# Optimization experiments

Hardware: AMD Instinct MI355X
Metric: run time of the kernel (lower is better)

Reference implementation:

```python
import jax, jax.numpy as jnp
import numpy as np

VAT_TOKENS = 57
ACTION_NUM = 56
NUM_HEADS = 16
DIM = 1152
HEAD_DIM = DIM // NUM_HEADS
SCALE = HEAD_DIM ** -0.5
N_GROUPS = 3  # num_non_act = 768 -> 3 groups of 256


def setup_inputs() -> dict:
    key = jax.random.key(0)
    ks = jax.random.split(key, 8)
    B, N, C = 32, VAT_TOKENS + 768, DIM
    w_std = C ** -0.5
    return {
        "x": jax.random.normal(ks[0], (B, N, C), jnp.float32),
        "w_qkv_non": jax.random.normal(ks[1], (3 * C, C), jnp.float32) * w_std,
        "w_q_act": jax.random.normal(ks[2], (C, C), jnp.float32) * w_std,
        "w_kv_act": jax.random.normal(ks[3], (2 * C, C), jnp.float32) * w_std,
        "w_proj_non": jax.random.normal(ks[4], (C, C), jnp.float32) * w_std,
        "b_proj_non": jnp.zeros((C,), jnp.float32),
        "w_proj_act": jax.random.normal(ks[5], (C, C), jnp.float32) * w_std,
        "b_proj_act": jnp.zeros((C,), jnp.float32),
    }


def reference(x, w_qkv_non, w_q_act, w_kv_act, w_proj_non, b_proj_non,
              w_proj_act, b_proj_act):
    B, N, C = x.shape
    H, Dh = NUM_HEADS, HEAD_DIM
    num_non_act = N - VAT_TOKENS
    G = num_non_act // N_GROUPS  # group size (256)

    # ---- non-action stream: windowed (grouped) self-attention ----
    non_act = x[:, VAT_TOKENS:]                                  # (B, 768, C)
    qkv = non_act @ w_qkv_non.T                                  # (B, 768, 3C)
    qkv = qkv.reshape(B, N_GROUPS, G, 3, H, Dh)
    q = qkv[:, :, :, 0]                                          # (B, g, G, H, Dh)
    k = qkv[:, :, :, 1]
    v = qkv[:, :, :, 2]
    attn = jnp.einsum('bgqhd,bgkhd->bghqk', q, k) * SCALE
    attn = jax.nn.softmax(attn, axis=-1)
    x_non = jnp.einsum('bghqk,bgkhd->bgqhd', attn, v)
    x_non = x_non.reshape(B, num_non_act, C)

    # ---- action stream: act queries attend to x[ACTION_NUM:] ----
    act = x[:, :VAT_TOKENS]
    q_act = (act @ w_q_act.T).reshape(B, VAT_TOKENS, H, Dh)
    kv = (x @ w_kv_act.T).reshape(B, N, 2, H, Dh)
    k_act = kv[:, ACTION_NUM:, 0]                                # (B, N-56, H, Dh)
    v_act = kv[:, ACTION_NUM:, 1]
    attn_act = jnp.einsum('bqhd,bkhd->bhqk', q_act, k_act) * SCALE
    attn_act = jax.nn.softmax(attn_act, axis=-1)
    x_act = jnp.einsum('bhqk,bkhd->bqhd', attn_act, v_act)
    x_act = x_act.reshape(B, VAT_TOKENS, C)

    # ---- output projections + concat ----
    x_non = x_non @ w_proj_non.T + b_proj_non
    x_act = x_act @ w_proj_act.T + b_proj_act
    return jnp.concatenate([x_act, x_non], axis=1)
```

## Files before the change

kernel.cpp:

```cpp
#include <hip/hip_runtime.h>

typedef __attribute__((ext_vector_type(8))) __bf16 bf16x8;
typedef __attribute__((ext_vector_type(4))) float f32x4;
typedef __attribute__((ext_vector_type(4))) unsigned short u16x4;
typedef __attribute__((ext_vector_type(8))) unsigned short u16x8;

#define MFMA_BF16 __builtin_amdgcn_mfma_f32_16x16x32_bf16

__device__ __forceinline__ unsigned short f2bf(float f) {
  union { float f; unsigned u; } v; v.f = f;
  unsigned r = v.u + 0x7FFFu + ((v.u >> 16) & 1u);
  return (unsigned short)(r >> 16);
}

__device__ __forceinline__ void gload16(const void* g, void* l) {
  __builtin_amdgcn_global_load_lds(
      (const __attribute__((address_space(1))) unsigned int*)g,
      (__attribute__((address_space(3))) unsigned int*)l, 16, 0, 0);
}

__global__ void __launch_bounds__(256) cast_bf16_kernel(const float* __restrict__ in,
                                                        unsigned short* __restrict__ out,
                                                        int n8) {
  int i = blockIdx.x * 256 + threadIdx.x;
  if (i >= n8) return;
  long base = (long)i * 8;
  float4 a = *(const float4*)(in + base);
  float4 b = *(const float4*)(in + base + 4);
  u16x8 o;
  o[0] = f2bf(a.x); o[1] = f2bf(a.y); o[2] = f2bf(a.z); o[3] = f2bf(a.w);
  o[4] = f2bf(b.x); o[5] = f2bf(b.y); o[6] = f2bf(b.z); o[7] = f2bf(b.w);
  *(u16x8*)(out + base) = o;
}

template <int REMAP>
__device__ __forceinline__ long remap_row(int m) {
  if (REMAP == 1) { int b = m / 768; return (long)b * 825 + 57 + (m - b * 768); }
  if (REMAP == 2) { int b = m / 57;  return (long)b * 825 + (m - b * 57); }
  return m;
}

template <int REMAP, bool PROJ>
__global__ void __launch_bounds__(512, 2) gemm256(const unsigned short* __restrict__ A,
                                                  const unsigned short* __restrict__ Bw,
                                                  void* __restrict__ Cout,
                                                  const float* __restrict__ bias,
                                                  int M, int N) {
  const int K = 1152;
  __shared__ unsigned short L[65536];
  unsigned short* Al = L;
  unsigned short* Bl = L + 32768;
  int tid = threadIdx.x;
  int lane = tid & 63;
  int wid = tid >> 6;
  int l15 = lane & 15, hi = lane >> 4;
  int wm = wid >> 2, wn = wid & 3;

  int gx = gridDim.x;
  int nwg = gx * gridDim.y;
  int orig = blockIdx.y * gx + blockIdx.x;
  int q8 = nwg >> 3, r8 = nwg & 7;
  int xcd = orig & 7, off = orig >> 3;
  int wgid = (xcd < r8 ? xcd * (q8 + 1) : r8 * (q8 + 1) + (xcd - r8) * q8) + off;
  int bn = wgid % gx, bm = wgid / gx;
  int m0 = bm * 256, n0 = bn * 256;

  int rlo = tid >> 2;
  int cg = ((tid & 3) - (tid >> 3)) & 3;
  int ma0 = m0 + rlo;       if (ma0 > M - 1) ma0 = M - 1;
  int ma1 = m0 + rlo + 128; if (ma1 > M - 1) ma1 = M - 1;
  const unsigned short* aptr0 = A + remap_row<REMAP>(ma0) * K + cg * 8;
  const unsigned short* aptr1 = A + remap_row<REMAP>(ma1) * K + cg * 8;
  int nb0 = n0 + rlo;       if (nb0 > N - 1) nb0 = N - 1;
  int nb1 = n0 + rlo + 128; if (nb1 > N - 1) nb1 = N - 1;
  const unsigned short* bptr0 = Bw + (long)nb0 * K + cg * 8;
  const unsigned short* bptr1 = Bw + (long)nb1 * K + cg * 8;
  unsigned ldst = (unsigned)tid * 8;

  unsigned short* Ad = Al + ldst;
  unsigned short* Bd = Bl + ldst;

  const int cl = (hi + (l15 >> 1)) & 3;
  const unsigned short* arb[4];
  const unsigned short* brb[4];
#pragma unroll
  for (int f = 0; f < 4; ++f) {
    arb[f] = Al + (wm * 128 + f * 16 + l15) * 32 + cl * 8;
    brb[f] = Bl + (wn * 64 + f * 16 + l15) * 32 + cl * 8;
  }

#define STAGE(P)                                                        \
  {                                                                     \
    gload16(aptr0 + (P) * 32, Ad + (((P) & 3) << 13));                  \
    gload16(aptr1 + (P) * 32, Ad + ((((P) & 3) << 13)) + 4096);         \
    gload16(bptr0 + (P) * 32, Bd + (((P) & 3) << 13));                  \
    gload16(bptr1 + (P) * 32, Bd + ((((P) & 3) << 13)) + 4096);         \
  }
#define READ_FA(P, S)                                                   \
  {                                                                     \
    _Pragma("unroll") for (int f = 0; f < 8; ++f)                       \
        fA[S][f] = *(const bf16x8*)(arb[f & 3] + (((P) & 3) << 13) + (f >> 2) * 2048); \
  }
#define READ_FB(P)                                                      \
  {                                                                     \
    _Pragma("unroll") for (int f = 0; f < 4; ++f)                       \
        fB[f] = *(const bf16x8*)(brb[f] + (((P) & 3) << 13));           \
  }

  STAGE(0); STAGE(1); STAGE(2);
  __builtin_amdgcn_sched_barrier(0);
  asm volatile("s_waitcnt vmcnt(4)" ::: "memory");
  __builtin_amdgcn_s_barrier();
  __builtin_amdgcn_sched_barrier(0);

  bf16x8 fA[2][8];
  bf16x8 fB[4];
  READ_FA(0, 0);
  READ_FB(0);
  f32x4 acc[8][4] = {};

#pragma unroll
  for (int p = 0; p < 36; ++p) {
    const int cur = p & 1;
    if (p < 35) READ_FA(p + 1, cur ^ 1);
    __builtin_amdgcn_sched_barrier(0);
    __builtin_amdgcn_s_setprio(1);
#pragma unroll
    for (int fm = 0; fm < 8; ++fm)
#pragma unroll
      for (int fn = 0; fn < 4; ++fn)
        acc[fm][fn] = MFMA_BF16(fA[cur][fm], fB[fn], acc[fm][fn], 0, 0, 0);
    __builtin_amdgcn_s_setprio(0);
    if (p < 35) READ_FB(p + 1);
    if (p <= 32) STAGE(p + 3);
    if (p <= 32)      asm volatile("s_waitcnt vmcnt(4)" ::: "memory");
    else if (p == 33) asm volatile("s_waitcnt vmcnt(0)" ::: "memory");
    if (p < 35) {
      __builtin_amdgcn_sched_barrier(0);
      __builtin_amdgcn_s_barrier();
      __builtin_amdgcn_sched_barrier(0);
    }
  }
#undef STAGE
#undef READ_FA
#undef READ_FB

  if (!PROJ) {
    unsigned short* reg = L + wid * 8192;
#pragma unroll
    for (int a = 0; a < 8; ++a) {
#pragma unroll
      for (int fn = 0; fn < 4; ++fn) {
        int rbase = a * 16 + hi * 4;
#pragma unroll
        for (int r = 0; r < 4; ++r) {
          int row = rbase + r;
          int ch = (fn * 2 + (l15 >> 3)) ^ (row & 7);
          reg[row * 64 + ch * 8 + (l15 & 7)] = f2bf(acc[a][fn][r]);
        }
      }
    }
#pragma unroll
    for (int i = 0; i < 16; ++i) {
      int rr = i * 8 + (lane >> 3);
      int ch = (lane & 7) ^ (rr & 7);
      u16x8 v = *(const u16x8*)(reg + rr * 64 + ch * 8);
      int m = m0 + wm * 128 + rr;
      int n = n0 + wn * 64 + (lane & 7) * 8;
      if (m < M && n < N)
        *(u16x8*)((unsigned short*)Cout + (long)m * N + n) = v;
    }
  } else {
    float* regf = (float*)L + wid * 4096;
    float bv[4];
#pragma unroll
    for (int fn = 0; fn < 4; ++fn) {
      int n = n0 + wn * 64 + fn * 16 + l15;
      bv[fn] = bias[n < N ? n : N - 1];
    }
#pragma unroll
    for (int half = 0; half < 2; ++half) {
#pragma unroll
      for (int a4 = 0; a4 < 4; ++a4) {
#pragma unroll
        for (int fn = 0; fn < 4; ++fn) {
          int rbase = a4 * 16 + hi * 4;
#pragma unroll
          for (int r = 0; r < 4; ++r)
            regf[(rbase + r) * 64 + fn * 16 + l15] = acc[half * 4 + a4][fn][r] + bv[fn];
        }
      }
#pragma unroll
      for (int i = 0; i < 16; ++i) {
        int rr = i * 4 + (lane >> 4);
        int cc = (lane & 15) * 4;
        f32x4 v = *(const f32x4*)(regf + rr * 64 + cc);
        int m = m0 + wm * 128 + half * 64 + rr;
        int n = n0 + wn * 64 + cc;
        if (m < M && n < N)
          *(f32x4*)((float*)Cout + remap_row<REMAP>(m) * N + n) = v;
      }
      if (half == 0) asm volatile("s_waitcnt lgkmcnt(0)" ::: "memory");
    }
  }
}

template <int REMAP, bool PROJ>
__global__ void __launch_bounds__(256) gemm_bt(const unsigned short* __restrict__ A,
                                               const unsigned short* __restrict__ Bw,
                                               void* __restrict__ Cout,
                                               const float* __restrict__ bias,
                                               int M, int N) {
  const int K = 1152;
  __shared__ unsigned short At[128 * 64];
  __shared__ unsigned short Bt[128 * 64];
  int tid = threadIdx.x;
  int lane = tid & 63, wid = tid >> 6;
  int l15 = lane & 15, hi = lane >> 4;
  int wm = wid >> 1, wn = wid & 1;
  int m0 = blockIdx.y * 128, n0 = blockIdx.x * 128;

  const unsigned short* asrc[4];
  const unsigned short* bsrc[4];
  unsigned ldsoff[4];
#pragma unroll
  for (int j = 0; j < 4; j++) {
    int c = tid + j * 256;
    int r = c >> 3;
    int cc = (c & 7) ^ (r & 7);
    ldsoff[j] = (unsigned)c * 8;
    int ma = m0 + r; if (ma > M - 1) ma = M - 1;
    asrc[j] = A + remap_row<REMAP>(ma) * K + cc * 8;
    bsrc[j] = Bw + (long)(n0 + r) * K + cc * 8;
  }

  f32x4 acc[4][4] = {};

  for (int kt = 0; kt < K; kt += 64) {
#pragma unroll
    for (int j = 0; j < 4; j++) {
      gload16(asrc[j] + kt, &At[ldsoff[j]]);
      gload16(bsrc[j] + kt, &Bt[ldsoff[j]]);
    }
    __syncthreads();
#pragma unroll
    for (int ks = 0; ks < 2; ks++) {
      bf16x8 af[4], bfr[4];
#pragma unroll
      for (int i = 0; i < 4; i++) {
        int ra = wm * 64 + i * 16 + l15;
        int ca = (ks * 64 + hi * 16) ^ ((ra & 7) << 4);
        af[i] = *(const bf16x8*)((const char*)At + ra * 128 + ca);
        int rb = wn * 64 + i * 16 + l15;
        int cb = (ks * 64 + hi * 16) ^ ((rb & 7) << 4);
        bfr[i] = *(const bf16x8*)((const char*)Bt + rb * 128 + cb);
      }
#pragma unroll
      for (int i = 0; i < 4; i++)
#pragma unroll
        for (int j = 0; j < 4; j++)
          acc[i][j] = MFMA_BF16(af[i], bfr[j], acc[i][j], 0, 0, 0);
    }
    __syncthreads();
  }

#pragma unroll
  for (int j = 0; j < 4; j++) {
    int n = n0 + wn * 64 + j * 16 + l15;
    float bv = 0.f;
    if (PROJ) bv = bias[n];
#pragma unroll
    for (int i = 0; i < 4; i++) {
      int mb = m0 + wm * 64 + i * 16 + hi * 4;
#pragma unroll
      for (int r = 0; r < 4; r++) {
        int m = mb + r;
        if (m < M) {
          if (PROJ)
            ((float*)Cout)[remap_row<REMAP>(m) * N + n] = acc[i][j][r] + bv;
          else
            ((unsigned short*)Cout)[(long)m * N + n] = f2bf(acc[i][j][r]);
        }
      }
    }
  }
}

__global__ void __launch_bounds__(256) attn_non(const unsigned short* __restrict__ qkv,
                                                unsigned short* __restrict__ o) {
  int h = blockIdx.x, g = blockIdx.y, b = blockIdx.z;
  __shared__ unsigned short K_s[128 * 104];
  __shared__ unsigned short V_s[80 * 136];
  __shared__ unsigned short P_s[16 * 16 * 40];
  int tid = threadIdx.x, lane = tid & 63, wid = tid >> 6;
  int l15 = lane & 15, hi = lane >> 4;
  const long base = (long)((b * 3 + g) * 256) * 3456;
  const float SC2 = 0.11785113019775793f * 1.4426950408889634f;

  bf16x8 qf[4][3];
#pragma unroll
  for (int qt = 0; qt < 4; qt++)
#pragma unroll
    for (int ds = 0; ds < 3; ds++) {
      int q = wid * 64 + qt * 16 + l15;
      int d = ds * 32 + hi * 8;
      if (d < 72)
        qf[qt][ds] = *(const bf16x8*)(qkv + base + (long)q * 3456 + h * 72 + d);
      else {
        u16x8 z = {0, 0, 0, 0, 0, 0, 0, 0};
        qf[qt][ds] = __builtin_bit_cast(bf16x8, z);
      }
    }

  f32x4 ot[5][4] = {};
  float lsum[4] = {0.f, 0.f, 0.f, 0.f};

  for (int c0 = 0; c0 < 256; c0 += 128) {
    {
      int r = tid >> 1, hf = tid & 1;
      const unsigned short* src = qkv + base + (long)(c0 + r) * 3456 + (16 + h) * 72 + hf * 48;
      unsigned short* dst = &K_s[r * 104 + hf * 48];
#pragma unroll
      for (int j = 0; j < 6; j++) {
        int col = hf * 48 + j * 8;
        u16x8 v = {0, 0, 0, 0, 0, 0, 0, 0};
        if (col < 72) v = *(const u16x8*)(src + j * 8);
        *(u16x8*)(dst + j * 8) = v;
      }
    }
    if (tid < 128) {
      const unsigned short* src = qkv + base + (long)(c0 + tid) * 3456 + (32 + h) * 72;
      u16x8 w[9];
#pragma unroll
      for (int j = 0; j < 9; j++) w[j] = *(const u16x8*)(src + j * 8);
#pragma unroll
      for (int j = 0; j < 9; j++)
#pragma unroll
        for (int e = 0; e < 8; e++) V_s[(j * 8 + e) * 136 + tid] = w[j][e];
    }
    __syncthreads();

#pragma unroll
    for (int k32 = 0; k32 < 4; k32++) {
#pragma unroll
      for (int kt = 0; kt < 2; kt++) {
        bf16x8 kf[3];
#pragma unroll
        for (int ds = 0; ds < 3; ds++)
          kf[ds] = *(const bf16x8*)((const char*)K_s +
                     ((k32 * 32 + kt * 16 + l15) * 104 + ds * 32 + hi * 8) * 2);
#pragma unroll
        for (int qt = 0; qt < 4; qt++) {
          f32x4 st = {};
#pragma unroll
          for (int ds = 0; ds < 3; ds++) st = MFMA_BF16(kf[ds], qf[qt][ds], st, 0, 0, 0);
          u16x4 pw;
#pragma unroll
          for (int r = 0; r < 4; r++) {
            float p = exp2f(st[r] * SC2);
            lsum[qt] += p;
            pw[r] = f2bf(p);
          }
          *(u16x4*)&P_s[((wid * 4 + qt) * 16 + l15) * 40 + kt * 16 + hi * 4] = pw;
        }
      }
      bf16x8 pf[4];
#pragma unroll
      for (int qt = 0; qt < 4; qt++)
        pf[qt] = *(const bf16x8*)&P_s[((wid * 4 + qt) * 16 + l15) * 40 + hi * 8];
#pragma unroll
      for (int dt = 0; dt < 5; dt++) {
        bf16x8 vf = *(const bf16x8*)&V_s[(dt * 16 + l15) * 136 + k32 * 32 + hi * 8];
#pragma unroll
        for (int qt = 0; qt < 4; qt++) ot[dt][qt] = MFMA_BF16(vf, pf[qt], ot[dt][qt], 0, 0, 0);
      }
    }
    __syncthreads();
  }

#pragma unroll
  for (int qt = 0; qt < 4; qt++) {
    float s = lsum[qt];
    s += __shfl_xor(s, 16);
    s += __shfl_xor(s, 32);
    lsum[qt] = 1.0f / s;
  }
#pragma unroll
  for (int dt = 0; dt < 5; dt++)
#pragma unroll
    for (int qt = 0; qt < 4; qt++)
#pragma unroll
      for (int r = 0; r < 4; r++) {
        int d = dt * 16 + hi * 4 + r;
        if (d < 72) {
          long row = (long)b * 825 + 57 + g * 256 + wid * 64 + qt * 16 + l15;
          o[row * 1152 + h * 72 + d] = f2bf(ot[dt][qt][r] * lsum[qt]);
        }
      }
}

__global__ void __launch_bounds__(256) attn_act(const unsigned short* __restrict__ kv,
                                                const unsigned short* __restrict__ qa,
                                                unsigned short* __restrict__ o) {
  int h = blockIdx.x, b = blockIdx.y;
  __shared__ unsigned short K_s[128 * 104];
  __shared__ unsigned short V_s[80 * 136];
  __shared__ unsigned short P_s[4 * 16 * 40];
  int tid = threadIdx.x, lane = tid & 63, wid = tid >> 6;
  int l15 = lane & 15, hi = lane >> 4;
  const float SC2 = 0.11785113019775793f * 1.4426950408889634f;
  const int LIM = 769;

  bf16x8 qf[3];
  {
    int q = wid * 16 + l15; if (q > 56) q = 56;
#pragma unroll
    for (int ds = 0; ds < 3; ds++) {
      int d = ds * 32 + hi * 8;
      if (d < 72)
        qf[ds] = *(const bf16x8*)(qa + (long)(b * 57 + q) * 1152 + h * 72 + d);
      else {
        u16x8 z = {0, 0, 0, 0, 0, 0, 0, 0};
        qf[ds] = __builtin_bit_cast(bf16x8, z);
      }
    }
  }

  f32x4 ot[5] = {};
  float lsum = 0.f;
  const long kbase = (long)b * 825 + 56;

  for (int c0 = 0; c0 < LIM; c0 += 128) {
    int valid = LIM - c0; if (valid > 128) valid = 128;
    {
      int r = tid >> 1, hf = tid & 1;
      int rr = r < valid ? r : valid - 1;
      const unsigned short* src = kv + (kbase + c0 + rr) * 2304 + h * 72 + hf * 48;
      unsigned short* dst = &K_s[r * 104 + hf * 48];
#pragma unroll
      for (int j = 0; j < 6; j++) {
        int col = hf * 48 + j * 8;
        u16x8 v = {0, 0, 0, 0, 0, 0, 0, 0};
        if (col < 72) v = *(const u16x8*)(src + j * 8);
        *(u16x8*)(dst + j * 8) = v;
      }
    }
    if (tid < 128) {
      int rr = tid < valid ? tid : valid - 1;
      const unsigned short* src = kv + (kbase + c0 + rr) * 2304 + (16 + h) * 72;
      u16x8 w[9];
#pragma unroll
      for (int j = 0; j < 9; j++) w[j] = *(const u16x8*)(src + j * 8);
#pragma unroll
      for (int j = 0; j < 9; j++)
#pragma unroll
        for (int e = 0; e < 8; e++) V_s[(j * 8 + e) * 136 + tid] = w[j][e];
    }
    __syncthreads();

#pragma unroll
    for (int k32 = 0; k32 < 4; k32++) {
#pragma unroll
      for (int kt = 0; kt < 2; kt++) {
        bf16x8 kf[3];
#pragma unroll
        for (int ds = 0; ds < 3; ds++)
          kf[ds] = *(const bf16x8*)((const char*)K_s +
                     ((k32 * 32 + kt * 16 + l15) * 104 + ds * 32 + hi * 8) * 2);
        f32x4 st = {};
#pragma unroll
        for (int ds = 0; ds < 3; ds++) st = MFMA_BF16(kf[ds], qf[ds], st, 0, 0, 0);
        u16x4 pw;
#pragma unroll
        for (int r = 0; r < 4; r++) {
          int kg = c0 + k32 * 32 + kt * 16 + hi * 4 + r;
          float p = (kg < LIM) ? exp2f(st[r] * SC2) : 0.f;
          lsum += p;
          pw[r] = f2bf(p);
        }
        *(u16x4*)&P_s[(wid * 16 + l15) * 40 + kt * 16 + hi * 4] = pw;
      }
      bf16x8 pf = *(const bf16x8*)&P_s[(wid * 16 + l15) * 40 + hi * 8];
#pragma unroll
      for (int dt = 0; dt < 5; dt++) {
        bf16x8 vf = *(const bf16x8*)&V_s[(dt * 16 + l15) * 136 + k32 * 32 + hi * 8];
        ot[dt] = MFMA_BF16(vf, pf, ot[dt], 0, 0, 0);
      }
    }
    __syncthreads();
  }

  {
    float s = lsum;
    s += __shfl_xor(s, 16);
    s += __shfl_xor(s, 32);
    lsum = 1.0f / s;
  }
  int q = wid * 16 + l15;
#pragma unroll
  for (int dt = 0; dt < 5; dt++)
#pragma unroll
    for (int r = 0; r < 4; r++) {
      int d = dt * 16 + hi * 4 + r;
      if (d < 72 && q < 57)
        o[((long)b * 825 + q) * 1152 + h * 72 + d] = f2bf(ot[dt][r] * lsum);
    }
}

extern "C" void kernel_launch(void* const* d_in, const int* in_sizes, int n_in,
                              void* d_out, int out_size, void* d_ws, size_t ws_size,
                              hipStream_t stream) {
  const float* x     = (const float*)d_in[0];
  const float* w_qkv = (const float*)d_in[1];
  const float* w_q   = (const float*)d_in[2];
  const float* w_kv  = (const float*)d_in[3];
  const float* w_pn  = (const float*)d_in[4];
  const float* b_pn  = (const float*)d_in[5];
  const float* w_pa  = (const float*)d_in[6];
  const float* b_pa  = (const float*)d_in[7];

  char* ws = (char*)d_ws;
  unsigned short* xb    = (unsigned short*)ws; ws += (size_t)26400 * 1152 * 2;
  unsigned short* wqkvb = (unsigned short*)ws; ws += (size_t)3456 * 1152 * 2;
  unsigned short* wqb   = (unsigned short*)ws; ws += (size_t)1152 * 1152 * 2;
  unsigned short* wkvb  = (unsigned short*)ws; ws += (size_t)2304 * 1152 * 2;
  unsigned short* wpnb  = (unsigned short*)ws; ws += (size_t)1152 * 1152 * 2;
  unsigned short* wpab  = (unsigned short*)ws; ws += (size_t)1152 * 1152 * 2;
  unsigned short* qkvw  = (unsigned short*)ws; ws += (size_t)24576 * 3456 * 2;
  unsigned short* kvw   = (unsigned short*)ws; ws += (size_t)26400 * 2304 * 2;
  unsigned short* qw    = (unsigned short*)ws; ws += (size_t)1824 * 1152 * 2;
  unsigned short* attnw = (unsigned short*)ws; ws += (size_t)26400 * 1152 * 2;

  auto cast = [&](const float* src, unsigned short* dst, long n) {
    int n8 = (int)(n / 8);
    cast_bf16_kernel<<<(n8 + 255) / 256, 256, 0, stream>>>(src, dst, n8);
  };
  cast(x,     xb,    26400L * 1152);
  cast(w_qkv, wqkvb, 3456L * 1152);
  cast(w_q,   wqb,   1152L * 1152);
  cast(w_kv,  wkvb,  2304L * 1152);
  cast(w_pn,  wpnb,  1152L * 1152);
  cast(w_pa,  wpab,  1152L * 1152);

  gemm256<1, false><<<dim3(14, 96), 512, 0, stream>>>(xb, wqkvb, qkvw, nullptr, 24576, 3456);
  gemm256<0, false><<<dim3(9, 104), 512, 0, stream>>>(xb, wkvb, kvw, nullptr, 26400, 2304);
  gemm_bt<2, false><<<dim3(9, 15), 256, 0, stream>>>(xb, wqb, qw, nullptr, 1824, 1152);

  attn_non<<<dim3(16, 3, 32), 256, 0, stream>>>(qkvw, attnw);
  attn_act<<<dim3(16, 32), 256, 0, stream>>>(kvw, qw, attnw);

  gemm256<1, true><<<dim3(5, 96), 512, 0, stream>>>(attnw, wpnb, d_out, b_pn, 24576, 1152);
  gemm_bt<2, true><<<dim3(9, 15), 256, 0, stream>>>(attnw, wpab, d_out, b_pa, 1824, 1152);
}
```

Before: 737.0 us.

## Merge casts and GEMMs into grouped kernels to cut launches and tail waste

New measurement: 672.0 us. -8.8%, faster.

```diff
diff --git a/kernel.cpp b/kernel.cpp
--- a/kernel.cpp
+++ b/kernel.cpp
@@ -19,12 +19,9 @@
       (__attribute__((address_space(3))) unsigned int*)l, 16, 0, 0);
 }
 
-__global__ void __launch_bounds__(256) cast_bf16_kernel(const float* __restrict__ in,
-                                                        unsigned short* __restrict__ out,
-                                                        int n8) {
-  int i = blockIdx.x * 256 + threadIdx.x;
-  if (i >= n8) return;
-  long base = (long)i * 8;
+__device__ __forceinline__ void cast8(const float* __restrict__ in,
+                                      unsigned short* __restrict__ out, long i) {
+  long base = i * 8;
   float4 a = *(const float4*)(in + base);
   float4 b = *(const float4*)(in + base + 4);
   u16x8 o;
@@ -33,6 +30,25 @@
   *(u16x8*)(out + base) = o;
 }
 
+__global__ void __launch_bounds__(256) cast_all(
+    const float* __restrict__ x, const float* __restrict__ wqkv,
+    const float* __restrict__ wq, const float* __restrict__ wkv,
+    const float* __restrict__ wpn, const float* __restrict__ wpa,
+    unsigned short* __restrict__ xb, unsigned short* __restrict__ wqkvb,
+    unsigned short* __restrict__ wqb, unsigned short* __restrict__ wkvb,
+    unsigned short* __restrict__ wpnb, unsigned short* __restrict__ wpab) {
+  const long c0 = 3801600, c1 = 4299264, c2 = 4465152, c3 = 4796928,
+             c4 = 4962816, c5 = 5128704;
+  long i = (long)blockIdx.x * 256 + threadIdx.x;
+  if (i >= c5) return;
+  if (i < c0)      cast8(x,    xb,    i);
+  else if (i < c1) cast8(wqkv, wqkvb, i - c0);
+  else if (i < c2) cast8(wq,   wqb,   i - c1);
+  else if (i < c3) cast8(wkv,  wkvb,  i - c2);
+  else if (i < c4) cast8(wpn,  wpnb,  i - c3);
+  else             cast8(wpa,  wpab,  i - c4);
+}
+
 template <int REMAP>
 __device__ __forceinline__ long remap_row(int m) {
   if (REMAP == 1) { int b = m / 768; return (long)b * 825 + 57 + (m - b * 768); }
@@ -41,13 +57,13 @@
 }
 
 template <int REMAP, bool PROJ>
-__global__ void __launch_bounds__(512, 2) gemm256(const unsigned short* __restrict__ A,
-                                                  const unsigned short* __restrict__ Bw,
-                                                  void* __restrict__ Cout,
-                                                  const float* __restrict__ bias,
-                                                  int M, int N) {
+__device__ __forceinline__ void gemm_body(unsigned short* L, int orig, int gx, int nwg,
+                                          const unsigned short* __restrict__ A,
+                                          const unsigned short* __restrict__ Bw,
+                                          void* __restrict__ Cout,
+                                          const float* __restrict__ bias,
+                                          int M, int N) {
   const int K = 1152;
-  __shared__ unsigned short L[65536];
   unsigned short* Al = L;
   unsigned short* Bl = L + 32768;
   int tid = threadIdx.x;
@@ -56,9 +72,6 @@
   int l15 = lane & 15, hi = lane >> 4;
   int wm = wid >> 2, wn = wid & 3;
 
-  int gx = gridDim.x;
-  int nwg = gx * gridDim.y;
-  int orig = blockIdx.y * gx + blockIdx.x;
   int q8 = nwg >> 3, r8 = nwg & 7;
   int xcd = orig & 7, off = orig >> 3;
   int wgid = (xcd < r8 ? xcd * (q8 + 1) : r8 * (q8 + 1) + (xcd - r8) * q8) + off;
@@ -205,85 +218,31 @@
   }
 }
 
-template <int REMAP, bool PROJ>
-__global__ void __launch_bounds__(256) gemm_bt(const unsigned short* __restrict__ A,
-                                               const unsigned short* __restrict__ Bw,
-                                               void* __restrict__ Cout,
-                                               const float* __restrict__ bias,
-                                               int M, int N) {
-  const int K = 1152;
-  __shared__ unsigned short At[128 * 64];
-  __shared__ unsigned short Bt[128 * 64];
-  int tid = threadIdx.x;
-  int lane = tid & 63, wid = tid >> 6;
-  int l15 = lane & 15, hi = lane >> 4;
-  int wm = wid >> 1, wn = wid & 1;
-  int m0 = blockIdx.y * 128, n0 = blockIdx.x * 128;
-
-  const unsigned short* asrc[4];
-  const unsigned short* bsrc[4];
-  unsigned ldsoff[4];
-#pragma unroll
-  for (int j = 0; j < 4; j++) {
-    int c = tid + j * 256;
-    int r = c >> 3;
-    int cc = (c & 7) ^ (r & 7);
-    ldsoff[j] = (unsigned)c * 8;
-    int ma = m0 + r; if (ma > M - 1) ma = M - 1;
-    asrc[j] = A + remap_row<REMAP>(ma) * K + cc * 8;
-    bsrc[j] = Bw + (long)(n0 + r) * K + cc * 8;
-  }
-
-  f32x4 acc[4][4] = {};
-
-  for (int kt = 0; kt < K; kt += 64) {
-#pragma unroll
-    for (int j = 0; j < 4; j++) {
-      gload16(asrc[j] + kt, &At[ldsoff[j]]);
-      gload16(bsrc[j] + kt, &Bt[ldsoff[j]]);
-    }
-    __syncthreads();
-#pragma unroll
-    for (int ks = 0; ks < 2; ks++) {
-      bf16x8 af[4], bfr[4];
-#pragma unroll
-      for (int i = 0; i < 4; i++) {
-        int ra = wm * 64 + i * 16 + l15;
-        int ca = (ks * 64 + hi * 16) ^ ((ra & 7) << 4);
-        af[i] = *(const bf16x8*)((const char*)At + ra * 128 + ca);
-        int rb = wn * 64 + i * 16 + l15;
-        int cb = (ks * 64 + hi * 16) ^ ((rb & 7) << 4);
-        bfr[i] = *(const bf16x8*)((const char*)Bt + rb * 128 + cb);
-      }
-#pragma unroll
-      for (int i = 0; i < 4; i++)
-#pragma unroll
-        for (int j = 0; j < 4; j++)
-          acc[i][j] = MFMA_BF16(af[i], bfr[j], acc[i][j], 0, 0, 0);
-    }
-    __syncthreads();
-  }
-
-#pragma unroll
-  for (int j = 0; j < 4; j++) {
-    int n = n0 + wn * 64 + j * 16 + l15;
-    float bv = 0.f;
-    if (PROJ) bv = bias[n];
-#pragma unroll
-    for (int i = 0; i < 4; i++) {
-      int mb = m0 + wm * 64 + i * 16 + hi * 4;
-#pragma unroll
-      for (int r = 0; r < 4; r++) {
-        int m = mb + r;
-        if (m < M) {
-          if (PROJ)
-            ((float*)Cout)[remap_row<REMAP>(m) * N + n] = acc[i][j][r] + bv;
-          else
-            ((unsigned short*)Cout)[(long)m * N + n] = f2bf(acc[i][j][r]);
-        }
-      }
-    }
-  }
+__global__ void __launch_bounds__(512, 2) gemm_front(
+    const unsigned short* __restrict__ xb, const unsigned short* __restrict__ wqkvb,
+    const unsigned short* __restrict__ wkvb, const unsigned short* __restrict__ wqb,
+    unsigned short* __restrict__ qkvw, unsigned short* __restrict__ kvw,
+    unsigned short* __restrict__ qw) {
+  __shared__ unsigned short L[65536];
+  int bid = blockIdx.x;
+  if (bid < 1344)
+    gemm_body<1, false>(L, bid, 14, 1344, xb, wqkvb, qkvw, nullptr, 24576, 3456);
+  else if (bid < 2280)
+    gemm_body<0, false>(L, bid - 1344, 9, 936, xb, wkvb, kvw, nullptr, 26400, 2304);
+  else
+    gemm_body<2, false>(L, bid - 2280, 5, 40, xb, wqb, qw, nullptr, 1824, 1152);
+}
+
+__global__ void __launch_bounds__(512, 2) gemm_proj(
+    const unsigned short* __restrict__ attnw, const unsigned short* __restrict__ wpnb,
+    const unsigned short* __restrict__ wpab, float* __restrict__ out,
+    const float* __restrict__ bpn, const float* __restrict__ bpa) {
+  __shared__ unsigned short L[65536];
+  int bid = blockIdx.x;
+  if (bid < 480)
+    gemm_body<1, true>(L, bid, 5, 480, attnw, wpnb, out, bpn, 24576, 1152);
+  else
+    gemm_body<2, true>(L, bid - 480, 5, 40, attnw, wpab, out, bpa, 1824, 1152);
 }
 
 __global__ void __launch_bounds__(256) attn_non(const unsigned short* __restrict__ qkv,
@@ -531,24 +490,13 @@
   unsigned short* qw    = (unsigned short*)ws; ws += (size_t)1824 * 1152 * 2;
   unsigned short* attnw = (unsigned short*)ws; ws += (size_t)26400 * 1152 * 2;
 
-  auto cast = [&](const float* src, unsigned short* dst, long n) {
-    int n8 = (int)(n / 8);
-    cast_bf16_kernel<<<(n8 + 255) / 256, 256, 0, stream>>>(src, dst, n8);
-  };
-  cast(x,     xb,    26400L * 1152);
-  cast(w_qkv, wqkvb, 3456L * 1152);
-  cast(w_q,   wqb,   1152L * 1152);
-  cast(w_kv,  wkvb,  2304L * 1152);
-  cast(w_pn,  wpnb,  1152L * 1152);
-  cast(w_pa,  wpab,  1152L * 1152);
-
-  gemm256<1, false><<<dim3(14, 96), 512, 0, stream>>>(xb, wqkvb, qkvw, nullptr, 24576, 3456);
-  gemm256<0, false><<<dim3(9, 104), 512, 0, stream>>>(xb, wkvb, kvw, nullptr, 26400, 2304);
-  gemm_bt<2, false><<<dim3(9, 15), 256, 0, stream>>>(xb, wqb, qw, nullptr, 1824, 1152);
+  cast_all<<<20034, 256, 0, stream>>>(x, w_qkv, w_q, w_kv, w_pn, w_pa,
+                                      xb, wqkvb, wqb, wkvb, wpnb, wpab);
+
+  gemm_front<<<2320, 512, 0, stream>>>(xb, wqkvb, wkvb, wqb, qkvw, kvw, qw);
 
   attn_non<<<dim3(16, 3, 32), 256, 0, stream>>>(qkvw, attnw);
   attn_act<<<dim3(16, 32), 256, 0, stream>>>(kvw, qw, attnw);
 
-  gemm256<1, true><<<dim3(5, 96), 512, 0, stream>>>(attnw, wpnb, d_out, b_pn, 24576, 1152);
-  gemm_bt<2, true><<<dim3(9, 15), 256, 0, stream>>>(attnw, wpab, d_out, b_pa, 1824, 1152);
-}
+  gemm_proj<<<520, 512, 0, stream>>>(attnw, wpnb, wpab, (float*)d_out, b_pn, b_pa);
+}
```
